# Kernel tuning notes

Measured on AMD Instinct MI355X. Metric: run time of the kernel, lower is better.

Reference implementation:

```python
import jax, jax.numpy as jnp
import numpy as np

D = 512      # d_x
H = 8        # n_I
DH = 64      # d_q = d_k = d_v = d_r
L = 4        # n_L
NUM_KNOTS = 5
ORDER = 3
KNOTS = np.linspace(-1.0, 1.0, NUM_KNOTS + ORDER)  # 8 uniform knots
EPS = 1e-5


def layernorm(x, w, b):
    mu = jnp.mean(x, axis=-1, keepdims=True)
    var = jnp.mean((x - mu) ** 2, axis=-1, keepdims=True)
    return (x - mu) * jax.lax.rsqrt(var + EPS) * w + b


def bspline_basis(x):
    # Cox-de Boor recursion on uniform knots, vectorized over all knot indices.
    # x: [...]; returns [..., len(KNOTS)-1-ORDER] = [..., 4]
    t = KNOTS
    B = jnp.stack([((t[k] <= x) & (x < t[k + 1])).astype(x.dtype)
                   for k in range(len(t) - 1)], axis=-1)
    for m in range(1, ORDER + 1):
        cols = []
        for k in range(len(t) - 1 - m):
            left = (x - t[k]) / (t[k + m] - t[k]) * B[..., k]
            right = (t[k + m + 1] - x) / (t[k + m + 1] - t[k + 1]) * B[..., k + 1]
            cols.append(left + right)
        B = jnp.stack(cols, axis=-1)
    return B


def setup_inputs() -> dict:
    key = jax.random.key(0)
    ks = jax.random.split(key, 20)
    B_, S = 4, 1024
    inp = {
        "src": jax.random.normal(ks[0], (B_, S, D), dtype=jnp.float32),
        "ln1_w": jnp.ones((L, D)), "ln1_b": jnp.zeros((L, D)),
        "ln2_w": jnp.ones((L, D)), "ln2_b": jnp.zeros((L, D)),
        "ln3_w": jnp.ones((L, D)), "ln3_b": jnp.zeros((L, D)),
        "Wq_w": jax.random.normal(ks[1], (L, H * DH, D)) * 0.02,
        "Wq_b": jnp.zeros((L, H * DH)),
        "Wk_w": jax.random.normal(ks[2], (L, H * DH, D)) * 0.02,
        "Wk_b": jnp.zeros((L, H * DH)),
        "Wv_w": jax.random.normal(ks[3], (L, H * DH, D)) * 0.02,
        "Wv_b": jnp.zeros((L, H * DH)),
        "Wr_w": jax.random.normal(ks[4], (L, H * DH, D)) * (1.0 / np.sqrt(DH)),
        "Wr_b": jnp.zeros((L, H * DH)),
        "Wo_w": jax.random.normal(ks[5], (L, D, H * DH)) * 0.02,
        "Wo_b": jnp.zeros((L, D)),
        "inner_c": jax.random.normal(ks[6], (L, D, NUM_KNOTS)) * 0.1,
        "outer_c": jax.random.normal(ks[7], (L, D, D)) * 0.1,
        "src_mask": jnp.ones((B_, 1, 1, S), dtype=jnp.int32),
    }
    return inp


def reference(src, ln1_w, ln1_b, ln2_w, ln2_b, ln3_w, ln3_b,
              Wq_w, Wq_b, Wk_w, Wk_b, Wv_w, Wv_b, Wr_w, Wr_b, Wo_w, Wo_b,
              inner_c, outer_c, src_mask):
    bsz, S, _ = src.shape
    scale = 1.0 / np.sqrt(DH)
    for l in range(L):
        # --- self-attention block ---
        z = layernorm(src, ln1_w[l], ln1_b[l])
        def heads(W, b):
            return (z @ W.T + b).reshape(bsz, S, H, DH).transpose(0, 2, 1, 3)
        Q = heads(Wq_w[l], Wq_b[l])
        K = heads(Wk_w[l], Wk_b[l])
        V = heads(Wv_w[l], Wv_b[l])
        R = heads(Wr_w[l], Wr_b[l])
        dot = jnp.einsum('bhid,bhjd->bhij', Q, K) * scale
        dot = jnp.where(src_mask == 0, -1e10, dot)
        att = jax.nn.softmax(dot, axis=-1)
        v_bar = jnp.einsum('bhjd,bhij->bhid', V, att)
        new_v = (v_bar * R).transpose(0, 2, 1, 3).reshape(bsz, S, H * DH)
        src = src + new_v @ Wo_w[l].T + Wo_b[l]
        # --- KAN feedforward block ---
        z = layernorm(src, ln2_w[l], ln2_b[l])
        xt = jnp.tanh(z)
        basis = bspline_basis(xt)            # [b,s,D,4]
        nb = NUM_KNOTS - ORDER               # only first 2 basis fns used
        inner = jnp.einsum('bsdk,dk->bsd', basis[..., :nb], inner_c[l][:, :nb])
        out = jnp.einsum('bsd,od->bso', inner, outer_c[l])
        src = src + out
        src = layernorm(src, ln3_w[l], ln3_b[l])
    return src
```

## Files before the change

### kernel.cpp

```cpp
#include <hip/hip_runtime.h>

#define B_   4
#define S_   1024
#define D_   512
#define H_   8
#define DH_  64
#define L_   4
#define NTOK (B_ * S_)
#define NT   (NTOK * D_)
#define DD   (D_ * D_)

typedef __attribute__((ext_vector_type(8))) short bf16x8;
typedef __attribute__((ext_vector_type(4))) float f32x4;

#define GLL(gp, lp)                                                            \
    __builtin_amdgcn_global_load_lds(                                          \
        (const __attribute__((address_space(1))) unsigned int*)(gp),           \
        (__attribute__((address_space(3))) unsigned int*)(lp), 16, 0, 0)

__device__ __forceinline__ float us2f(unsigned short u) {
    unsigned int v = ((unsigned int)u) << 16;
    return __uint_as_float(v);
}
__device__ __forceinline__ unsigned short f2us(float f) {
    unsigned int u = __float_as_uint(f);
    unsigned int r = (u + 0x7fffu + ((u >> 16) & 1u)) >> 16;
    return (unsigned short)r;
}

__device__ __forceinline__ float tanh_fast(float z) {
    float zc = fminf(fmaxf(z, -20.f), 20.f);
    float e = __builtin_amdgcn_exp2f(zc * 2.8853900817779268f);
    return 1.f - 2.f * __builtin_amdgcn_rcpf(e + 1.f);
}

__device__ __forceinline__ float bspl3(float u) {
    float a = fabsf(u);
    float t2 = fmaxf(2.f - a, 0.f);
    float t1 = fmaxf(1.f - a, 0.f);
    float c2 = t2 * t2 * t2;
    float c1 = t1 * t1 * t1;
    return (c2 - 4.f * c1) * (1.f / 6.f);
}

__device__ __forceinline__ float kan_fast(float zv, float c0, float c1) {
    float xt = tanh_fast(zv);
    float b0 = bspl3(__builtin_fmaf(xt, 3.5f, 1.5f));
    float b1 = bspl3(__builtin_fmaf(xt, 3.5f, 0.5f));
    return c0 * b0 + c1 * b1;
}

struct PreArgs {
    const float* w[6];
    unsigned short* cw;
    const float* src;
    const float* ln1w;
    const float* ln1b;
    float* srcf;
    unsigned short* z;
};
__global__ __launch_bounds__(256) void pre_k(PreArgs a) {
    int bx = blockIdx.x;
    if (bx < 6144) {
        int y = bx >> 8;
        int l = y / 6, tp = y - l * 6;
        int i = ((bx & 255) * 256 + threadIdx.x) * 4;
        float4 v = *(const float4*)(a.w[tp] + (size_t)l * DD + i);
        ushort4 o;
        o.x = f2us(v.x); o.y = f2us(v.y); o.z = f2us(v.z); o.w = f2us(v.w);
        *(ushort4*)(a.cw + (size_t)y * DD + i) = o;
    } else {
        int wv = threadIdx.x >> 6, lane = threadIdx.x & 63;
        int tok = (bx - 6144) * 4 + wv;
        const float* xr = a.src + (size_t)tok * D_;
        float v[8];
        float s = 0.f, s2 = 0.f;
#pragma unroll
        for (int i = 0; i < 8; ++i) {
            float t = xr[lane + 64 * i];
            v[i] = t; s += t; s2 += t * t;
        }
#pragma unroll
        for (int o = 1; o < 64; o <<= 1) { s += __shfl_xor(s, o); s2 += __shfl_xor(s2, o); }
        float mu = s * (1.f / D_);
        float var = s2 * (1.f / D_) - mu * mu;
        float rs = rsqrtf(var + 1e-5f);
#pragma unroll
        for (int i = 0; i < 8; ++i) {
            int d = lane + 64 * i;
            a.srcf[(size_t)tok * D_ + d] = v[i];
            a.z[(size_t)tok * D_ + d] = f2us((v[i] - mu) * rs * a.ln1w[d] + a.ln1b[d]);
        }
    }
}

struct MGemm128Args {
    const unsigned short* A;
    const unsigned short* W[4];
    const float* bias[4];
    unsigned short* C[4];
    int tflag[4];
};

__global__ __launch_bounds__(256) void mgemm128_k(MGemm128Args g) {
    __shared__ unsigned short As[2][128 * 64];
    __shared__ unsigned short Bs[2][128 * 64];
    int id = blockIdx.x + (blockIdx.y << 2) + (blockIdx.z << 7);
    int id2 = ((id & 7) << 6) + (id >> 3);
    int z = id2 >> 7;
    const unsigned short* W = g.W[z];
    const float* bias = g.bias[z];
    unsigned short* C = g.C[z];
    int m0 = ((id2 >> 2) & 31) * 128, n0 = (id2 & 3) * 128;
    int t = threadIdx.x;
    int wave = t >> 6, lane = t & 63;
    int wm = (wave >> 1) * 64, wn = (wave & 1) * 64;
    int l15 = lane & 15, quad = lane >> 4;
    int srow = lane >> 3, schunk = lane & 7;

    f32x4 acc[4][4];
#pragma unroll
    for (int i = 0; i < 4; ++i)
#pragma unroll
        for (int j = 0; j < 4; ++j)
#pragma unroll
            for (int r = 0; r < 4; ++r) acc[i][j][r] = 0.f;

    int rb = wave * 32;
    int swz = l15 & 7;

    #define STAGE128(buf, k0)                                                       \
        do {                                                                        \
            _Pragma("unroll")                                                       \
            for (int g8 = 0; g8 < 4; ++g8) {                                        \
                int row0 = rb + g8 * 8;                                             \
                int row = row0 + srow;                                              \
                int cg = schunk ^ (row & 7);                                        \
                GLL(g.A + (size_t)(m0 + row) * D_ + (k0) + cg * 8, &As[buf][row0 * 64]); \
                GLL(W   + (size_t)(n0 + row) * D_ + (k0) + cg * 8, &Bs[buf][row0 * 64]); \
            }                                                                       \
        } while (0)

    STAGE128(0, 0);

    int cur = 0;
    for (int ks = 0; ks < 8; ++ks) {
        if (ks < 7) {
            STAGE128(cur ^ 1, (ks + 1) * 64);
            asm volatile("s_waitcnt vmcnt(8)" ::: "memory");
        } else {
            asm volatile("s_waitcnt vmcnt(0)" ::: "memory");
        }
        __builtin_amdgcn_s_barrier();
        __builtin_amdgcn_sched_barrier(0);
#pragma unroll
        for (int kc = 0; kc < 2; ++kc) {
            int ch = ((kc * 4 + quad) ^ swz) * 8;
            bf16x8 af[4], bfr[4];
#pragma unroll
            for (int mt = 0; mt < 4; ++mt)
                af[mt] = *(const bf16x8*)&As[cur][(wm + mt * 16 + l15) * 64 + ch];
#pragma unroll
            for (int nt = 0; nt < 4; ++nt)
                bfr[nt] = *(const bf16x8*)&Bs[cur][(wn + nt * 16 + l15) * 64 + ch];
#pragma unroll
            for (int mt = 0; mt < 4; ++mt)
#pragma unroll
                for (int nt = 0; nt < 4; ++nt)
                    acc[mt][nt] = __builtin_amdgcn_mfma_f32_16x16x32_bf16(
                        af[mt], bfr[nt], acc[mt][nt], 0, 0, 0);
        }
        __builtin_amdgcn_sched_barrier(0);
        __builtin_amdgcn_s_barrier();
        cur ^= 1;
    }
    #undef STAGE128

    if (g.tflag[z]) {
#pragma unroll
        for (int mt = 0; mt < 4; ++mt)
#pragma unroll
            for (int nt = 0; nt < 4; ++nt) {
                int n = n0 + wn + nt * 16 + l15;
                float bv = bias[n];
                int m = m0 + wm + mt * 16 + quad * 4;
                ushort4 pk;
                pk.x = f2us(acc[mt][nt][0] + bv);
                pk.y = f2us(acc[mt][nt][1] + bv);
                pk.z = f2us(acc[mt][nt][2] + bv);
                pk.w = f2us(acc[mt][nt][3] + bv);
                *(ushort4*)(C + ((size_t)(m >> 10) * 512 + n) * 1024 + (m & 1023)) = pk;
            }
    } else {
#pragma unroll
        for (int mt = 0; mt < 4; ++mt)
#pragma unroll
            for (int nt = 0; nt < 4; ++nt) {
                int n = n0 + wn + nt * 16 + l15;
                float bv = bias[n];
#pragma unroll
                for (int r = 0; r < 4; ++r) {
                    int m = m0 + wm + mt * 16 + quad * 4 + r;
                    C[(size_t)m * D_ + n] = f2us(acc[mt][nt][r] + bv);
                }
            }
    }
}

struct GFArgs {
    const unsigned short* A;
    const unsigned short* W1;
    const unsigned short* W2;
    const float* bias1;
    const float* res;
    float* srcf;
    float* outp;
    unsigned short* zb;
    const float* w2a; const float* b2a;
    const float* w3;  const float* b3;
    const float* w1n; const float* b1n;
    const float* ic;
};

template <int LAST>
__global__ __launch_bounds__(512) void gemmfused_k(GFArgs g) {
    __shared__ unsigned short Bs[2][512 * 64];
    __shared__ unsigned short As[16 * 512];
    __shared__ float redS[16][8];
    __shared__ float redS2[16][8];

    int m0 = blockIdx.x * 16;
    int t = threadIdx.x, wave = t >> 6, lane = t & 63;
    int l15 = lane & 15, quad = lane >> 4;
    int srow = lane >> 3, schunk = lane & 7;
    int swz = l15 & 7;

#pragma unroll
    for (int rr = 0; rr < 2; ++rr) {
        int r = wave * 2 + rr;
        GLL(g.A + (size_t)(m0 + r) * D_ + (lane ^ (r & 7)) * 8, &As[r * 512]);
    }
    const unsigned short* Wp1 = g.W1 + (size_t)(wave * 64 + srow) * D_ + (schunk ^ srow) * 8;
#pragma unroll
    for (int g8 = 0; g8 < 8; ++g8)
        GLL(Wp1 + (size_t)g8 * 8 * D_, &Bs[0][(wave * 64 + g8 * 8) * 64]);
#pragma unroll
    for (int g8 = 0; g8 < 8; ++g8)
        GLL(Wp1 + 64 + (size_t)g8 * 8 * D_, &Bs[1][(wave * 64 + g8 * 8) * 64]);
    asm volatile("s_waitcnt vmcnt(16)" ::: "memory");
    __builtin_amdgcn_s_barrier();

    #define KLOOP(accv, Wp)                                                           \
        for (int ks = 0; ks < 8; ++ks) {                                              \
            if (ks < 7) asm volatile("s_waitcnt vmcnt(8)" ::: "memory");              \
            else        asm volatile("s_waitcnt vmcnt(0)" ::: "memory");              \
            __builtin_amdgcn_sched_barrier(0);                                        \
            _Pragma("unroll")                                                         \
            for (int kc = 0; kc < 2; ++kc) {                                          \
                bf16x8 af = *(const bf16x8*)&As[l15 * 512 +                           \
                                                ((ks * 8 + kc * 4 + quad) ^ swz) * 8];\
                _Pragma("unroll")                                                     \
                for (int nt = 0; nt < 4; ++nt) {                                      \
                    bf16x8 bf = *(const bf16x8*)&Bs[ks & 1][(wave * 64 + nt * 16 + l15) * 64 + \
                                                            ((kc * 4 + quad) ^ swz) * 8];      \
                    accv[nt] = __builtin_amdgcn_mfma_f32_16x16x32_bf16(af, bf, accv[nt], 0, 0, 0); \
                }                                                                     \
            }                                                                         \
            __builtin_amdgcn_sched_barrier(0);                                        \
            if (ks < 6) {                                                             \
                _Pragma("unroll")                                                     \
                for (int g8 = 0; g8 < 8; ++g8)                                        \
                    GLL(Wp + (ks + 2) * 64 + (size_t)g8 * 8 * D_,                     \
                        &Bs[ks & 1][(wave * 64 + g8 * 8) * 64]);                      \
            }                                                                         \
        }

    #define ROWSTATS(vals, muv, rsv)                                                  \
        {                                                                             \
            __builtin_amdgcn_s_barrier();                                             \
            float s_[4] = {0.f, 0.f, 0.f, 0.f}, s2_[4] = {0.f, 0.f, 0.f, 0.f};        \
            _Pragma("unroll")                                                         \
            for (int nt = 0; nt < 4; ++nt)                                            \
                _Pragma("unroll")                                                     \
                for (int r = 0; r < 4; ++r) {                                         \
                    s_[r] += vals[nt][r]; s2_[r] += vals[nt][r] * vals[nt][r];        \
                }                                                                     \
            _Pragma("unroll")                                                         \
            for (int off = 1; off < 16; off <<= 1)                                    \
                _Pragma("unroll")                                                     \
                for (int r = 0; r < 4; ++r) {                                         \
                    s_[r] += __shfl_xor(s_[r], off); s2_[r] += __shfl_xor(s2_[r], off); \
                }                                                                     \
            if (l15 == 0) {                                                           \
                _Pragma("unroll")                                                     \
                for (int r = 0; r < 4; ++r) {                                         \
                    redS[quad * 4 + r][wave] = s_[r]; redS2[quad * 4 + r][wave] = s2_[r]; \
                }                                                                     \
            }                                                                         \
            asm volatile("s_waitcnt lgkmcnt(0)" ::: "memory");                        \
            __builtin_amdgcn_s_barrier();                                             \
            _Pragma("unroll")                                                         \
            for (int r = 0; r < 4; ++r) {                                             \
                float ss = 0.f, ss2 = 0.f;                                            \
                _Pragma("unroll")                                                     \
                for (int w = 0; w < 8; ++w) {                                         \
                    ss += redS[quad * 4 + r][w]; ss2 += redS2[quad * 4 + r][w];       \
                }                                                                     \
                muv[r] = ss * (1.f / D_);                                             \
                rsv[r] = rsqrtf(ss2 * (1.f / D_) - muv[r] * muv[r] + 1e-5f);          \
            }                                                                         \
        }

    f32x4 acc[4];
#pragma unroll
    for (int nt = 0; nt < 4; ++nt)
#pragma unroll
        for (int r = 0; r < 4; ++r) acc[nt][r] = 0.f;
    KLOOP(acc, Wp1)

    const unsigned short* Wp2 = g.W2 + (size_t)(wave * 64 + srow) * D_ + (schunk ^ srow) * 8;
#pragma unroll
    for (int g8 = 0; g8 < 8; ++g8)
        GLL(Wp2 + (size_t)g8 * 8 * D_, &Bs[0][(wave * 64 + g8 * 8) * 64]);
#pragma unroll
    for (int g8 = 0; g8 < 8; ++g8)
        GLL(Wp2 + 64 + (size_t)g8 * 8 * D_, &Bs[1][(wave * 64 + g8 * 8) * 64]);

    float c0v[4], c1v[4], w2v[4], b2v[4];
#pragma unroll
    for (int nt = 0; nt < 4; ++nt) {
        int n = wave * 64 + nt * 16 + l15;
        c0v[nt] = g.ic[n * 5 + 0];
        c1v[nt] = g.ic[n * 5 + 1];
        w2v[nt] = g.w2a[n];
        b2v[nt] = g.b2a[n];
    }

    float tv[4][4];
#pragma unroll
    for (int nt = 0; nt < 4; ++nt) {
        int n = wave * 64 + nt * 16 + l15;
        float bv = g.bias1[n];
#pragma unroll
        for (int r = 0; r < 4; ++r)
            tv[nt][r] = acc[nt][r] + bv + g.res[(size_t)(m0 + quad * 4 + r) * D_ + n];
    }

    float mu2[4], rs2[4];
    ROWSTATS(tv, mu2, rs2)

#pragma unroll
    for (int nt = 0; nt < 4; ++nt) {
        int n = wave * 64 + nt * 16 + l15;
        int gch = n >> 3;
#pragma unroll
        for (int r = 0; r < 4; ++r) {
            int row = quad * 4 + r;
            float zv = (tv[nt][r] - mu2[r]) * rs2[r] * w2v[nt] + b2v[nt];
            As[row * 512 + (gch ^ (row & 7)) * 8 + (n & 7)] =
                f2us(kan_fast(zv, c0v[nt], c1v[nt]));
        }
    }
    asm volatile("s_waitcnt lgkmcnt(0)" ::: "memory");
    __builtin_amdgcn_s_barrier();
    __builtin_amdgcn_sched_barrier(0);

    f32x4 acc2[4];
#pragma unroll
    for (int nt = 0; nt < 4; ++nt)
#pragma unroll
        for (int r = 0; r < 4; ++r) acc2[nt][r] = 0.f;
    KLOOP(acc2, Wp2)

    float tv2[4][4];
#pragma unroll
    for (int nt = 0; nt < 4; ++nt)
#pragma unroll
        for (int r = 0; r < 4; ++r) tv2[nt][r] = acc2[nt][r] + tv[nt][r];

    float mu3[4], rs3[4];
    ROWSTATS(tv2, mu3, rs3)

    float yv[4][4];
#pragma unroll
    for (int nt = 0; nt < 4; ++nt) {
        int n = wave * 64 + nt * 16 + l15;
#pragma unroll
        for (int r = 0; r < 4; ++r) {
            float v = (tv2[nt][r] - mu3[r]) * rs3[r] * g.w3[n] + g.b3[n];
            yv[nt][r] = v;
            if (LAST) g.outp[(size_t)(m0 + quad * 4 + r) * D_ + n] = v;
            else      g.srcf[(size_t)(m0 + quad * 4 + r) * D_ + n] = v;
        }
    }

    if (!LAST) {
        float mu1[4], rs1[4];
        ROWSTATS(yv, mu1, rs1)
#pragma unroll
        for (int nt = 0; nt < 4; ++nt) {
            int n = wave * 64 + nt * 16 + l15;
#pragma unroll
            for (int r = 0; r < 4; ++r)
                g.zb[(size_t)(m0 + quad * 4 + r) * D_ + n] =
                    f2us((yv[nt][r] - mu1[r]) * rs1[r] * g.w1n[n] + g.b1n[n]);
        }
    }
    #undef KLOOP
    #undef ROWSTATS
}

__global__ __launch_bounds__(256) void attn_k(const unsigned short* __restrict__ Q,
                                              const unsigned short* __restrict__ K,
                                              const unsigned short* __restrict__ vt,
                                              const unsigned short* __restrict__ R,
                                              const int* __restrict__ mask,
                                              unsigned short* __restrict__ O) {
    __shared__ unsigned short Ks[2][64 * 64];
    __shared__ unsigned short Vts[2][64 * 64];
    __shared__ unsigned short Ps[4][16][72];
    __shared__ float Ms[1024];

    int bh = blockIdx.x;
    int b = bh >> 3, h = bh & 7;
    int qt0 = blockIdx.y * 64;
    int t = threadIdx.x, wave = t >> 6, lane = t & 63;
    int l15 = lane & 15, quad = lane >> 4;
    int qw0 = qt0 + wave * 16;

    const unsigned short* Qrow = Q + ((size_t)(b * S_ + qw0 + l15) * H_ + h) * DH_;
    bf16x8 qf[2];
    qf[0] = *(const bf16x8*)(Qrow + quad * 8);
    qf[1] = *(const bf16x8*)(Qrow + 32 + quad * 8);

#pragma unroll
    for (int u = 0; u < 4; ++u)
        Ms[u * 256 + t] = mask[b * S_ + u * 256 + t] ? 0.f : -1e10f;
    asm volatile("s_waitcnt lgkmcnt(0)" ::: "memory");

    float lsum = 0.f;
    f32x4 acc_o[4];
#pragma unroll
    for (int dt = 0; dt < 4; ++dt)
#pragma unroll
        for (int r = 0; r < 4; ++r) acc_o[dt][r] = 0.f;

    int lro = lane >> 3;
    int cglob = (lane & 7) ^ lro;
    const unsigned short* kgp0 =
        K + ((size_t)(b * S_ + wave * 16 + lro) * H_ + h) * DH_ + cglob * 8;
    const unsigned short* vgp0 =
        vt + (size_t)(b * 512 + h * 64 + wave * 16 + lro) * 1024 + cglob * 8;
    int swz = l15 & 7;
    const float SC = 0.125f * 1.44269504089f;

    #define ASTAGE(buf, kt)                                                         \
        do {                                                                        \
            GLL(kgp0 + (size_t)(kt) * 64 * 512,           &Ks[buf][(wave * 16) * 64]);     \
            GLL(kgp0 + (size_t)(kt) * 64 * 512 + 8 * 512, &Ks[buf][(wave * 16 + 8) * 64]); \
            GLL(vgp0 + (kt) * 64,                         &Vts[buf][(wave * 16) * 64]);    \
            GLL(vgp0 + (kt) * 64 + 8 * 1024,              &Vts[buf][(wave * 16 + 8) * 64]);\
        } while (0)

    ASTAGE(0, 0);

    int cur = 0;
    for (int kt = 0; kt < 16; ++kt) {
        if (kt < 15) {
            ASTAGE(cur ^ 1, kt + 1);
            asm volatile("s_waitcnt vmcnt(4)" ::: "memory");
        } else {
            asm volatile("s_waitcnt vmcnt(0)" ::: "memory");
        }
        __builtin_amdgcn_s_barrier();
        __builtin_amdgcn_sched_barrier(0);

        f32x4 accs[4];
#pragma unroll
        for (int jt = 0; jt < 4; ++jt)
#pragma unroll
            for (int r = 0; r < 4; ++r) accs[jt][r] = 0.f;
        __builtin_amdgcn_s_setprio(1);
#pragma unroll
        for (int kc = 0; kc < 2; ++kc) {
            int ch = ((kc * 4 + quad) ^ swz) * 8;
#pragma unroll
            for (int jt = 0; jt < 4; ++jt) {
                bf16x8 kf = *(const bf16x8*)&Ks[cur][(jt * 16 + l15) * 64 + ch];
                accs[jt] = __builtin_amdgcn_mfma_f32_16x16x32_bf16(kf, qf[kc], accs[jt], 0, 0, 0);
            }
        }
        __builtin_amdgcn_s_setprio(0);

#pragma unroll
        for (int jt = 0; jt < 4; ++jt) {
            int kb = kt * 64 + jt * 16 + quad * 4;
            float p0 = __builtin_amdgcn_exp2f(accs[jt][0] * SC + Ms[kb + 0]);
            float p1 = __builtin_amdgcn_exp2f(accs[jt][1] * SC + Ms[kb + 1]);
            float p2 = __builtin_amdgcn_exp2f(accs[jt][2] * SC + Ms[kb + 2]);
            float p3 = __builtin_amdgcn_exp2f(accs[jt][3] * SC + Ms[kb + 3]);
            lsum += (p0 + p1) + (p2 + p3);
            uint2 pk;
            pk.x = __builtin_amdgcn_perm(__float_as_uint(p1), __float_as_uint(p0), 0x07060302u);
            pk.y = __builtin_amdgcn_perm(__float_as_uint(p3), __float_as_uint(p2), 0x07060302u);
            *(uint2*)&Ps[wave][l15][jt * 16 + quad * 4] = pk;
        }

        __builtin_amdgcn_s_setprio(1);
#pragma unroll
        for (int kc = 0; kc < 2; ++kc) {
            bf16x8 pf = *(const bf16x8*)&Ps[wave][l15][kc * 32 + quad * 8];
            int ch = ((kc * 4 + quad) ^ swz) * 8;
#pragma unroll
            for (int dt = 0; dt < 4; ++dt) {
                bf16x8 vf = *(const bf16x8*)&Vts[cur][(dt * 16 + l15) * 64 + ch];
                acc_o[dt] = __builtin_amdgcn_mfma_f32_16x16x32_bf16(pf, vf, acc_o[dt], 0, 0, 0);
            }
        }
        __builtin_amdgcn_s_setprio(0);

        __builtin_amdgcn_sched_barrier(0);
        __builtin_amdgcn_s_barrier();
        cur ^= 1;
    }
    #undef ASTAGE

    lsum += __shfl_xor(lsum, 16);
    lsum += __shfl_xor(lsum, 32);

#pragma unroll
    for (int r = 0; r < 4; ++r) {
        int qq = quad * 4 + r;
        int q = qw0 + qq;
        float inv = 1.f / __shfl(lsum, qq);
        const unsigned short* Rr = R + ((size_t)(b * S_ + q) * H_ + h) * DH_;
        unsigned short* Or = O + ((size_t)(b * S_ + q) * H_ + h) * DH_;
#pragma unroll
        for (int dt = 0; dt < 4; ++dt) {
            int d = dt * 16 + l15;
            Or[d] = f2us(acc_o[dt][r] * inv * us2f(Rr[d]));
        }
    }
}

extern "C" void kernel_launch(void* const* d_in, const int* in_sizes, int n_in,
                              void* d_out, int out_size, void* d_ws, size_t ws_size,
                              hipStream_t stream) {
    const float* src  = (const float*)d_in[0];
    const float* ln1w = (const float*)d_in[1];
    const float* ln1b = (const float*)d_in[2];
    const float* ln2w = (const float*)d_in[3];
    const float* ln2b = (const float*)d_in[4];
    const float* ln3w = (const float*)d_in[5];
    const float* ln3b = (const float*)d_in[6];
    const float* wq   = (const float*)d_in[7];
    const float* wqb  = (const float*)d_in[8];
    const float* wk   = (const float*)d_in[9];
    const float* wkb  = (const float*)d_in[10];
    const float* wv   = (const float*)d_in[11];
    const float* wvb  = (const float*)d_in[12];
    const float* wr   = (const float*)d_in[13];
    const float* wrb  = (const float*)d_in[14];
    const float* wo   = (const float*)d_in[15];
    const float* wob  = (const float*)d_in[16];
    const float* ic   = (const float*)d_in[17];
    const float* oc   = (const float*)d_in[18];
    const int* mask   = (const int*)d_in[19];
    float* out = (float*)d_out;

    float* srcf = (float*)d_ws;
    unsigned short* zb = (unsigned short*)(srcf + NT);
    unsigned short* qb = zb + NT;
    unsigned short* kb = qb + NT;
    unsigned short* vb = kb + NT;
    unsigned short* rb = vb + NT;
    unsigned short* cw = rb + NT;

    PreArgs pa;
    pa.w[0] = wq; pa.w[1] = wk; pa.w[2] = wv;
    pa.w[3] = wr; pa.w[4] = wo; pa.w[5] = oc;
    pa.cw = cw; pa.src = src; pa.ln1w = ln1w; pa.ln1b = ln1b;
    pa.srcf = srcf; pa.z = zb;
    pre_k<<<dim3(6144 + NTOK / 4), dim3(256), 0, stream>>>(pa);

    for (int l = 0; l < L_; ++l) {
        unsigned short* cwl = cw + (size_t)l * 6 * DD;

        MGemm128Args ga;
        ga.A = zb;
        ga.W[0] = cwl + 0 * DD; ga.bias[0] = wqb + l * D_; ga.C[0] = qb; ga.tflag[0] = 0;
        ga.W[1] = cwl + 1 * DD; ga.bias[1] = wkb + l * D_; ga.C[1] = kb; ga.tflag[1] = 0;
        ga.W[2] = cwl + 2 * DD; ga.bias[2] = wvb + l * D_; ga.C[2] = vb; ga.tflag[2] = 1;
        ga.W[3] = cwl + 3 * DD; ga.bias[3] = wrb + l * D_; ga.C[3] = rb; ga.tflag[3] = 0;
        mgemm128_k<<<dim3(4, 32, 4), dim3(256), 0, stream>>>(ga);

        attn_k<<<dim3(32, 16), dim3(256), 0, stream>>>(qb, kb, vb, rb, mask, zb);

        GFArgs gf;
        gf.A = zb; gf.W1 = cwl + 4 * DD; gf.W2 = cwl + 5 * DD;
        gf.bias1 = wob + l * D_; gf.res = srcf;
        gf.srcf = srcf; gf.outp = out; gf.zb = zb;
        gf.w2a = ln2w + l * D_; gf.b2a = ln2b + l * D_;
        gf.w3 = ln3w + l * D_; gf.b3 = ln3b + l * D_;
        gf.w1n = (l < L_ - 1) ? ln1w + (l + 1) * D_ : nullptr;
        gf.b1n = (l < L_ - 1) ? ln1b + (l + 1) * D_ : nullptr;
        gf.ic = ic + (size_t)l * D_ * 5;

        if (l < L_ - 1)
            gemmfused_k<0><<<dim3(NTOK / 16), dim3(512), 0, stream>>>(gf);
        else
            gemmfused_k<1><<<dim3(NTOK / 16), dim3(512), 0, stream>>>(gf);
    }
}
```

Measured before the change: 352.4 us.

## Load fused-GEMM weight fragments directly into registers instead of staging through LDS

The fused Wo+KAN GEMM kernel no longer stages weight tiles through a 128KB double-buffered LDS area with global_load_lds. Each wave now reads its B fragments straight from global memory into a 4-stage register ring. The second weight matrix is prefetched during the layernorm/KAN epilogue. The smaller LDS footprint and launch_bounds(512,2) permit two blocks per CU, at the cost of uncoalesced 16-byte global reads, much higher register pressure, and no LDS reuse of the weights.

```diff
diff --git a/kernel.cpp b/kernel.cpp
--- a/kernel.cpp
+++ b/kernel.cpp
@@ -223,56 +223,59 @@
 };
 
 template <int LAST>
-__global__ __launch_bounds__(512) void gemmfused_k(GFArgs g) {
-    __shared__ unsigned short Bs[2][512 * 64];
-    __shared__ unsigned short As[16 * 512];
+__global__ __launch_bounds__(512, 2) void gemmfused_k(GFArgs g) {
+    __shared__ unsigned short Asm[16 * 512];
     __shared__ float redS[16][8];
     __shared__ float redS2[16][8];
 
     int m0 = blockIdx.x * 16;
     int t = threadIdx.x, wave = t >> 6, lane = t & 63;
     int l15 = lane & 15, quad = lane >> 4;
-    int srow = lane >> 3, schunk = lane & 7;
     int swz = l15 & 7;
 
 #pragma unroll
     for (int rr = 0; rr < 2; ++rr) {
         int r = wave * 2 + rr;
-        GLL(g.A + (size_t)(m0 + r) * D_ + (lane ^ (r & 7)) * 8, &As[r * 512]);
-    }
-    const unsigned short* Wp1 = g.W1 + (size_t)(wave * 64 + srow) * D_ + (schunk ^ srow) * 8;
-#pragma unroll
-    for (int g8 = 0; g8 < 8; ++g8)
-        GLL(Wp1 + (size_t)g8 * 8 * D_, &Bs[0][(wave * 64 + g8 * 8) * 64]);
-#pragma unroll
-    for (int g8 = 0; g8 < 8; ++g8)
-        GLL(Wp1 + 64 + (size_t)g8 * 8 * D_, &Bs[1][(wave * 64 + g8 * 8) * 64]);
-    asm volatile("s_waitcnt vmcnt(16)" ::: "memory");
+        GLL(g.A + (size_t)(m0 + r) * D_ + (lane ^ (r & 7)) * 8, &Asm[r * 512]);
+    }
+    asm volatile("s_waitcnt vmcnt(0)" ::: "memory");
     __builtin_amdgcn_s_barrier();
 
-    #define KLOOP(accv, Wp)                                                           \
-        for (int ks = 0; ks < 8; ++ks) {                                              \
-            if (ks < 7) asm volatile("s_waitcnt vmcnt(8)" ::: "memory");              \
-            else        asm volatile("s_waitcnt vmcnt(0)" ::: "memory");              \
-            __builtin_amdgcn_sched_barrier(0);                                        \
-            _Pragma("unroll")                                                         \
-            for (int kc = 0; kc < 2; ++kc) {                                          \
-                bf16x8 af = *(const bf16x8*)&As[l15 * 512 +                           \
-                                                ((ks * 8 + kc * 4 + quad) ^ swz) * 8];\
-                _Pragma("unroll")                                                     \
-                for (int nt = 0; nt < 4; ++nt) {                                      \
-                    bf16x8 bf = *(const bf16x8*)&Bs[ks & 1][(wave * 64 + nt * 16 + l15) * 64 + \
-                                                            ((kc * 4 + quad) ^ swz) * 8];      \
-                    accv[nt] = __builtin_amdgcn_mfma_f32_16x16x32_bf16(af, bf, accv[nt], 0, 0, 0); \
-                }                                                                     \
-            }                                                                         \
-            __builtin_amdgcn_sched_barrier(0);                                        \
-            if (ks < 6) {                                                             \
-                _Pragma("unroll")                                                     \
-                for (int g8 = 0; g8 < 8; ++g8)                                        \
-                    GLL(Wp + (ks + 2) * 64 + (size_t)g8 * 8 * D_,                     \
-                        &Bs[ks & 1][(wave * 64 + g8 * 8) * 64]);                      \
-            }                                                                         \
+    const unsigned short* w1b = g.W1 + (size_t)(wave * 64 + l15) * D_ + quad * 8;
+    const unsigned short* w2b = g.W2 + (size_t)(wave * 64 + l15) * D_ + quad * 8;
+    #define WFRAG(b, nt, ks, kc) \
+        (*(const bf16x8*)((b) + (nt) * (16 * D_) + (ks) * 64 + (kc) * 32))
+
+    bf16x8 w[4][4][2];
+
+    #define WPRE(b)                                                    \
+        _Pragma("unroll")                                              \
+        for (int s = 0; s < 4; ++s)                                    \
+            _Pragma("unroll")                                          \
+            for (int nt = 0; nt < 4; ++nt)                             \
+                _Pragma("unroll")                                      \
+                for (int kc = 0; kc < 2; ++kc)                         \
+                    w[s][nt][kc] = WFRAG(b, nt, s, kc);
+
+    #define KLOOPR(accv, b)                                                            \
+        _Pragma("unroll")                                                              \
+        for (int ks = 0; ks < 8; ++ks) {                                               \
+            _Pragma("unroll")                                                          \
+            for (int kc = 0; kc < 2; ++kc) {                                           \
+                bf16x8 af = *(const bf16x8*)&Asm[l15 * 512 +                           \
+                                                 ((ks * 8 + kc * 4 + quad) ^ swz) * 8];\
+                _Pragma("unroll")                                                      \
+                for (int nt = 0; nt < 4; ++nt)                                         \
+                    accv[nt] = __builtin_amdgcn_mfma_f32_16x16x32_bf16(                \
+                        af, w[ks & 3][nt][kc], accv[nt], 0, 0, 0);                     \
+            }                                                                          \
+            if (ks < 4) {                                                              \
+                _Pragma("unroll")                                                      \
+                for (int nt = 0; nt < 4; ++nt)                                         \
+                    _Pragma("unroll")                                                  \
+                    for (int kc = 0; kc < 2; ++kc)                                     \
+                        w[ks & 3][nt][kc] = WFRAG(b, nt, ks + 4, kc);                  \
+            }                                                                          \
         }
 
     #define ROWSTATS(vals, muv, rsv)                                                  \
@@ -303,28 +306,21 @@
             for (int r = 0; r < 4; ++r) {                                             \
                 float ss = 0.f, ss2 = 0.f;                                            \
                 _Pragma("unroll")                                                     \
-                for (int w = 0; w < 8; ++w) {                                         \
-                    ss += redS[quad * 4 + r][w]; ss2 += redS2[quad * 4 + r][w];       \
+                for (int wv = 0; wv < 8; ++wv) {                                      \
+                    ss += redS[quad * 4 + r][wv]; ss2 += redS2[quad * 4 + r][wv];     \
                 }                                                                     \
                 muv[r] = ss * (1.f / D_);                                             \
                 rsv[r] = rsqrtf(ss2 * (1.f / D_) - muv[r] * muv[r] + 1e-5f);          \
             }                                                                         \
         }
 
+    WPRE(w1b)
     f32x4 acc[4];
 #pragma unroll
     for (int nt = 0; nt < 4; ++nt)
 #pragma unroll
         for (int r = 0; r < 4; ++r) acc[nt][r] = 0.f;
-    KLOOP(acc, Wp1)
-
-    const unsigned short* Wp2 = g.W2 + (size_t)(wave * 64 + srow) * D_ + (schunk ^ srow) * 8;
-#pragma unroll
-    for (int g8 = 0; g8 < 8; ++g8)
-        GLL(Wp2 + (size_t)g8 * 8 * D_, &Bs[0][(wave * 64 + g8 * 8) * 64]);
-#pragma unroll
-    for (int g8 = 0; g8 < 8; ++g8)
-        GLL(Wp2 + 64 + (size_t)g8 * 8 * D_, &Bs[1][(wave * 64 + g8 * 8) * 64]);
+    KLOOPR(acc, w1b)
 
     float c0v[4], c1v[4], w2v[4], b2v[4];
 #pragma unroll
@@ -349,6 +345,8 @@
     float mu2[4], rs2[4];
     ROWSTATS(tv, mu2, rs2)
 
+    WPRE(w2b)
+
 #pragma unroll
     for (int nt = 0; nt < 4; ++nt) {
         int n = wave * 64 + nt * 16 + l15;
@@ -357,20 +355,19 @@
         for (int r = 0; r < 4; ++r) {
             int row = quad * 4 + r;
             float zv = (tv[nt][r] - mu2[r]) * rs2[r] * w2v[nt] + b2v[nt];
-            As[row * 512 + (gch ^ (row & 7)) * 8 + (n & 7)] =
+            Asm[row * 512 + (gch ^ (row & 7)) * 8 + (n & 7)] =
                 f2us(kan_fast(zv, c0v[nt], c1v[nt]));
         }
     }
     asm volatile("s_waitcnt lgkmcnt(0)" ::: "memory");
     __builtin_amdgcn_s_barrier();
-    __builtin_amdgcn_sched_barrier(0);
 
     f32x4 acc2[4];
 #pragma unroll
     for (int nt = 0; nt < 4; ++nt)
 #pragma unroll
         for (int r = 0; r < 4; ++r) acc2[nt][r] = 0.f;
-    KLOOP(acc2, Wp2)
+    KLOOPR(acc2, w2b)
 
     float tv2[4][4];
 #pragma unroll
@@ -406,7 +403,9 @@
                     f2us((yv[nt][r] - mu1[r]) * rs1[r] * g.w1n[n] + g.b1n[n]);
         }
     }
-    #undef KLOOP
+    #undef KLOOPR
+    #undef WPRE
+    #undef WFRAG
     #undef ROWSTATS
 }
 
```

New measurement: 423.4 us. 20.2% more time.
